# Kernel tuning notes

Hardware: AMD Instinct MI355X
Metric: run time of the kernel (lower is better)

Reference implementation:

```python
import jax, jax.numpy as jnp
import numpy as np

D_MODEL = 1024
H = 16
DH = 64
FFN = 4096
CHUNK = 64
LN_EPS = 1e-5


def layer_norm(x, w, b):
    mu = x.mean(-1, keepdims=True)
    var = x.var(-1, keepdims=True)
    return (x - mu) * jax.lax.rsqrt(var + LN_EPS) * w + b


def l2_normalize(x):
    # matches torch F.normalize(p=2, dim=-1, eps=1e-12)
    n = jnp.sqrt(jnp.sum(x * x, axis=-1, keepdims=True))
    return x / jnp.maximum(n, 1e-12)


def chunk_gla(q, k, v, alpha, C=CHUNK):
    B, Hh, N, D = q.shape
    nc = N // C  # N chosen as multiple of C (pad==0 in original)
    q = q.reshape(B, Hh, nc, C, D)
    k = k.reshape(B, Hh, nc, C, D)
    v = v.reshape(B, Hh, nc, C, D)
    alpha = alpha.reshape(B, Hh, nc, C, D)

    log_a = jnp.log(jnp.maximum(alpha, 1e-6))
    la_cum = jnp.cumsum(log_a, axis=3)                  # (B,H,nc,C,D)
    la_mean = la_cum.mean(-1)                            # (B,H,nc,C)
    tril = jnp.tril(jnp.ones((C, C), dtype=q.dtype))
    decay = jnp.exp(la_mean[..., :, None] - la_mean[..., None, :]) * tril  # (B,H,nc,C,C)

    attn_intra = jnp.einsum('bhncd,bhnmd->bhncm', q, k) * decay
    o_intra = jnp.einsum('bhncm,bhnmd->bhncd', attn_intra, v)

    decay_to_end = jnp.exp(la_cum[:, :, :, -1:, :] - la_cum)
    kv_chunk = jnp.einsum('bhncf,bhnce->bhnfe', k * decay_to_end, v)  # (B,H,nc,D,D)
    chunk_decay = jnp.exp(log_a.sum(3))                  # (B,H,nc,D)
    q_dec = q * jnp.exp(la_cum)                          # decay_from_start

    def step(S, inp):
        qd, kv, cd = inp                                 # (B,H,C,D),(B,H,D,D),(B,H,D)
        o = jnp.einsum('bhcd,bhde->bhce', qd, S)
        S_new = S * cd[:, :, :, None] + kv
        return S_new, o

    S0 = jnp.zeros((B, Hh, D, D), dtype=q.dtype)
    _, o_inter = jax.lax.scan(
        step, S0,
        (jnp.moveaxis(q_dec, 2, 0), jnp.moveaxis(kv_chunk, 2, 0), jnp.moveaxis(chunk_decay, 2, 0)))
    o_inter = jnp.moveaxis(o_inter, 0, 2)                # (B,H,nc,C,D)
    return (o_intra + o_inter).reshape(B, Hh, N, D)


def setup_inputs() -> dict:
    key = jax.random.key(0)
    ks = jax.random.split(key, 16)
    s = 0.02
    td = H * DH
    return {
        'x': jax.random.normal(ks[0], (2, 4096, D_MODEL), dtype=jnp.float32),
        'Wq': jax.random.normal(ks[1], (D_MODEL, td), dtype=jnp.float32) * s,
        'Wk': jax.random.normal(ks[2], (D_MODEL, td), dtype=jnp.float32) * s,
        'Wv': jax.random.normal(ks[3], (D_MODEL, td), dtype=jnp.float32) * s,
        'Wg': jax.random.normal(ks[4], (D_MODEL, td), dtype=jnp.float32) * s,
        'bg': jnp.full((td,), -0.5, dtype=jnp.float32),
        'Wo': jax.random.normal(ks[5], (td, D_MODEL), dtype=jnp.float32) * s,
        'ln1_w': jnp.ones((D_MODEL,), jnp.float32),
        'ln1_b': jnp.zeros((D_MODEL,), jnp.float32),
        'ln2_w': jnp.ones((D_MODEL,), jnp.float32),
        'ln2_b': jnp.zeros((D_MODEL,), jnp.float32),
        'W1': jax.random.normal(ks[6], (D_MODEL, FFN), dtype=jnp.float32) * s,
        'b1': jnp.zeros((FFN,), jnp.float32),
        'W2': jax.random.normal(ks[7], (FFN, D_MODEL), dtype=jnp.float32) * s,
        'b2': jnp.zeros((D_MODEL,), jnp.float32),
    }


def reference(x, Wq, Wk, Wv, Wg, bg, Wo, ln1_w, ln1_b, ln2_w, ln2_b, W1, b1, W2, b2):
    B, N, _ = x.shape
    xn = layer_norm(x, ln1_w, ln1_b)
    q = (xn @ Wq).reshape(B, N, H, DH).transpose(0, 2, 1, 3)
    k = (xn @ Wk).reshape(B, N, H, DH).transpose(0, 2, 1, 3)
    v = (xn @ Wv).reshape(B, N, H, DH).transpose(0, 2, 1, 3)
    q = l2_normalize(q)
    k = l2_normalize(k)
    alpha = jax.nn.sigmoid(xn @ Wg + bg).reshape(B, N, H, DH).transpose(0, 2, 1, 3)
    o = chunk_gla(q, k, v, alpha)
    o = o.transpose(0, 2, 1, 3).reshape(B, N, H * DH)
    x = x + o @ Wo  # dropout off (eval / p=0)
    h = layer_norm(x, ln2_w, ln2_b)
    x = x + jax.nn.gelu(h @ W1 + b1, approximate=False) @ W2 + b2
    return x
```

## Files before the change

kernel.cpp:

```cpp
#include <hip/hip_runtime.h>

#define AS1 __attribute__((address_space(1)))
#define AS3 __attribute__((address_space(3)))

typedef unsigned short u16;
typedef short s16x8 __attribute__((ext_vector_type(8)));
typedef float f32x4 __attribute__((ext_vector_type(4)));
typedef float f32x16 __attribute__((ext_vector_type(16)));

__device__ __forceinline__ float bf2f(u16 u) {
    union { unsigned u; float f; } v; v.u = ((unsigned)u) << 16; return v.f;
}
__device__ __forceinline__ u16 f2bf(float f) {
    union { float f; unsigned u; } v; v.f = f;
    unsigned u = v.u;
    return (u16)((u + 0x7FFFu + ((u >> 16) & 1u)) >> 16);
}

__device__ __forceinline__ void gload16(const void* g, void* l) {
    __builtin_amdgcn_global_load_lds((const AS1 void*)g, (AS3 void*)l, 16, 0, 0);
}

__global__ __launch_bounds__(256) void transpose_bf16(
    const float* __restrict__ src, u16* __restrict__ dst, int R, int C)
{
    __shared__ float t[32][33];
    const int tx = threadIdx.x, ty = threadIdx.y;
    const int r0 = blockIdx.x * 32, c0 = blockIdx.y * 32;
#pragma unroll
    for (int i = 0; i < 4; i++)
        t[ty + i * 8][tx] = src[(size_t)(r0 + ty + i * 8) * C + c0 + tx];
    __syncthreads();
#pragma unroll
    for (int i = 0; i < 4; i++)
        dst[(size_t)(c0 + ty + i * 8) * R + r0 + tx] = f2bf(t[tx][ty + i * 8]);
}

__global__ __launch_bounds__(256) void ln_bf16(
    const float* __restrict__ x, const float* __restrict__ w,
    const float* __restrict__ b, u16* __restrict__ out)
{
    __shared__ float red[8];
    const int row = blockIdx.x;
    const int tid = threadIdx.x;
    const size_t base = (size_t)row * 1024 + tid * 4;
    const float4 xv = *(const float4*)&x[base];
    float s = xv.x + xv.y + xv.z + xv.w;
    float q = xv.x * xv.x + xv.y * xv.y + xv.z * xv.z + xv.w * xv.w;
#pragma unroll
    for (int m = 1; m < 64; m <<= 1) { s += __shfl_xor(s, m); q += __shfl_xor(q, m); }
    if ((tid & 63) == 0) { red[tid >> 6] = s; red[4 + (tid >> 6)] = q; }
    __syncthreads();
    s = red[0] + red[1] + red[2] + red[3];
    q = red[4] + red[5] + red[6] + red[7];
    const float mu = s * (1.f / 1024.f);
    const float var = q * (1.f / 1024.f) - mu * mu;
    const float rs = rsqrtf(var + 1e-5f);
    const float4 wv = *(const float4*)&w[tid * 4];
    const float4 bv = *(const float4*)&b[tid * 4];
    uint2 ov;
    ov.x = (unsigned)f2bf((xv.x - mu) * rs * wv.x + bv.x) |
           ((unsigned)f2bf((xv.y - mu) * rs * wv.y + bv.y) << 16);
    ov.y = (unsigned)f2bf((xv.z - mu) * rs * wv.z + bv.z) |
           ((unsigned)f2bf((xv.w - mu) * rs * wv.w + bv.w) << 16);
    *(uint2*)&out[base] = ov;
}

template <int EPX>
__global__ __launch_bounds__(256, 4) void gemm32(
    const u16* __restrict__ A, const u16* __restrict__ BT,
    float* __restrict__ Cf, u16* __restrict__ Cb,
    const float* __restrict__ bias, const float* __restrict__ resid,
    int M, int N, int K)
{
    __shared__ u16 As[2][4096];
    __shared__ u16 Bs[2][4096];
    const int tid = threadIdx.x;
    const int w = tid >> 6, l = tid & 63;
    const int tm = blockIdx.x * 128, tn = blockIdx.y * 128;
    const int wm = (w >> 1) * 64, wn = (w & 1) * 64;

    const int srow = l >> 2;
    const int sg = ((l & 3) ^ ((l >> 3) & 3)) * 8;
    size_t aSb[2], bSb[2];
#pragma unroll
    for (int j = 0; j < 2; j++) {
        aSb[j] = (size_t)(tm + w * 32 + j * 16 + srow) * K + sg;
        bSb[j] = (size_t)(tn + w * 32 + j * 16 + srow) * K + sg;
    }

    auto stage = [&](int t, int buf) {
        const int k0 = t * 32;
#pragma unroll
        for (int j = 0; j < 2; j++)
            gload16(&A[aSb[j] + k0], &As[buf][(w * 32 + j * 16) * 32]);
#pragma unroll
        for (int j = 0; j < 2; j++)
            gload16(&BT[bSb[j] + k0], &Bs[buf][(w * 32 + j * 16) * 32]);
    };

    const int hi = l >> 5;
    int aoff[2][2], boff[2][2];
#pragma unroll
    for (int mm = 0; mm < 2; mm++)
#pragma unroll
        for (int ks = 0; ks < 2; ks++) {
            const int ra = wm + mm * 32 + (l & 31);
            const int rb = wn + mm * 32 + (l & 31);
            const int key = ((l & 31) >> 1) & 3;
            aoff[mm][ks] = ra * 32 + ((ks * 2 + hi) ^ key) * 8;
            boff[mm][ks] = rb * 32 + ((ks * 2 + hi) ^ key) * 8;
        }

    f32x16 acc[2][2] = {};

    stage(0, 0);
    stage(1, 1);
    asm volatile("s_waitcnt vmcnt(4)" ::: "memory");
    __builtin_amdgcn_s_barrier();

    const int NT = K >> 5;
    for (int t = 0; t < NT; ++t) {
        const int buf = t & 1;
        const u16* as = As[buf];
        const u16* bs = Bs[buf];
        s16x8 a[2][2], b[2][2];
#pragma unroll
        for (int mm = 0; mm < 2; mm++)
#pragma unroll
            for (int ks = 0; ks < 2; ks++) {
                a[mm][ks] = *(const s16x8*)&as[aoff[mm][ks]];
                b[mm][ks] = *(const s16x8*)&bs[boff[mm][ks]];
            }
        asm volatile("s_waitcnt lgkmcnt(0)" ::: "memory");
        __builtin_amdgcn_sched_barrier(0);
        __builtin_amdgcn_s_barrier();
        const bool st = (t + 2 < NT);
        if (st) stage(t + 2, buf);
        __builtin_amdgcn_s_setprio(1);
#pragma unroll
        for (int ks = 0; ks < 2; ks++)
#pragma unroll
            for (int mm = 0; mm < 2; mm++)
#pragma unroll
                for (int nn = 0; nn < 2; nn++)
                    acc[mm][nn] = __builtin_amdgcn_mfma_f32_32x32x16_bf16(
                        a[mm][ks], b[nn][ks], acc[mm][nn], 0, 0, 0);
        __builtin_amdgcn_s_setprio(0);
        if (st)              asm volatile("s_waitcnt vmcnt(4)" ::: "memory");
        else if (t + 1 < NT) asm volatile("s_waitcnt vmcnt(0)" ::: "memory");
        __builtin_amdgcn_s_barrier();
    }

#pragma unroll
    for (int mm = 0; mm < 2; mm++)
#pragma unroll
        for (int nn = 0; nn < 2; nn++)
#pragma unroll
            for (int reg = 0; reg < 16; reg++) {
                const int row = tm + wm + mm * 32 + (l >> 5) * 4 + (reg & 3) + (reg >> 2) * 8;
                const int col = tn + wn + nn * 32 + (l & 31);
                const float v = acc[mm][nn][reg];
                if (EPX == 0) {
                    if (col < 3072) Cb[(size_t)row * 3072 + col] = f2bf(v);
                    else            Cf[(size_t)row * 1024 + (col - 3072)] = v;
                } else if (EPX == 1) {
                    const float u2 = v + bias[col];
                    Cb[(size_t)row * N + col] =
                        f2bf(0.5f * u2 * (1.f + erff(u2 * 0.70710678118654752f)));
                } else if (EPX == 2) {
                    const size_t idx = (size_t)row * N + col;
                    Cf[idx] = v + resid[idx];
                } else {
                    const size_t idx = (size_t)row * N + col;
                    Cf[idx] = v + bias[col] + resid[idx];
                }
            }
}

#define TP 72
#define LP 65
__global__ __launch_bounds__(256) void gla_a(
    const u16* __restrict__ qkv,
    const float* __restrict__ g,
    const float* __restrict__ bg,
    u16* __restrict__ qdec,
    u16* __restrict__ kvT,
    float* __restrict__ cdec,
    u16* __restrict__ ointra)
{
    __shared__ u16 Qh[64 * TP];
    __shared__ u16 Kh[64 * TP];
    __shared__ u16 VT[64 * TP];
    __shared__ float L[64 * LP];
    __shared__ float lm[64], nq[64], nk[64];

    const int bid = blockIdx.x;
    const int bh = bid >> 6, ck = bid & 63;
    const int b = bh >> 4, h = bh & 15;
    const int tok0 = b * 4096 + ck * 64;
    const int tid = threadIdx.x;
    const int w = tid >> 6, l = tid & 63;

#pragma unroll
    for (int pass = 0; pass < 2; pass++) {
        const int c = (tid >> 3) + pass * 32;
        const int col = (tid & 7) * 8;
        const size_t rb = (size_t)(tok0 + c) * 3072 + h * 64 + col;
        uint4 qv = *(const uint4*)&qkv[rb];
        uint4 kv_ = *(const uint4*)&qkv[rb + 1024];
        uint4 vv = *(const uint4*)&qkv[rb + 2048];
        *(uint4*)&Qh[c * TP + col] = qv;
        *(uint4*)&Kh[c * TP + col] = kv_;
        const u16* va = (const u16*)&vv;
#pragma unroll
        for (int j = 0; j < 8; j++) VT[(col + j) * TP + c] = va[j];
    }
#pragma unroll
    for (int pass = 0; pass < 4; pass++) {
        const int c = (tid >> 4) + pass * 16;
        const int col = (tid & 15) * 4;
        float4 gv = *(const float4*)&g[(size_t)(tok0 + c) * 1024 + h * 64 + col];
        float4 bgv = *(const float4*)&bg[h * 64 + col];
        const float* ga = (const float*)&gv;
        const float* ba = (const float*)&bgv;
#pragma unroll
        for (int i = 0; i < 4; i++) {
            const float z = ga[i] + ba[i];
            const float al = 1.f / (1.f + __expf(-z));
            L[c * LP + col + i] = __logf(fmaxf(al, 1e-6f));
        }
    }
    __syncthreads();

    {
        const int d = tid >> 2, qq = tid & 3;
        float vals[16];
#pragma unroll
        for (int i = 0; i < 16; i++) vals[i] = L[(qq * 16 + i) * LP + d];
        float s = 0.f;
#pragma unroll
        for (int i = 0; i < 16; i++) { s += vals[i]; vals[i] = s; }
        float sum = s;
        float u1 = __shfl_up(sum, 1, 4); if (qq >= 1) sum += u1;
        float u2 = __shfl_up(sum, 2, 4); if (qq >= 2) sum += u2;
        const float excl = sum - s;
#pragma unroll
        for (int i = 0; i < 16; i++) L[(qq * 16 + i) * LP + d] = vals[i] + excl;
        if (qq == 3) cdec[((size_t)bh * 64 + ck) * 64 + d] = __expf(sum);
    }
    __syncthreads();

    {
        const int c = tid >> 2, qq = tid & 3;
        float sl = 0.f, sq = 0.f, sk = 0.f;
        uint4 qa = *(const uint4*)&Qh[c * TP + qq * 16];
        uint4 qb = *(const uint4*)&Qh[c * TP + qq * 16 + 8];
        uint4 ka = *(const uint4*)&Kh[c * TP + qq * 16];
        uint4 kb = *(const uint4*)&Kh[c * TP + qq * 16 + 8];
        const u16* qu = (const u16*)&qa; const u16* qu2 = (const u16*)&qb;
        const u16* ku = (const u16*)&ka; const u16* ku2 = (const u16*)&kb;
#pragma unroll
        for (int i = 0; i < 8; i++) {
            float q1 = bf2f(qu[i]), q2 = bf2f(qu2[i]);
            float k1 = bf2f(ku[i]), k2 = bf2f(ku2[i]);
            sq += q1 * q1 + q2 * q2;
            sk += k1 * k1 + k2 * k2;
        }
#pragma unroll
        for (int i = 0; i < 16; i++) sl += L[c * LP + qq * 16 + i];
        sl += __shfl_xor(sl, 1); sl += __shfl_xor(sl, 2);
        sq += __shfl_xor(sq, 1); sq += __shfl_xor(sq, 2);
        sk += __shfl_xor(sk, 1); sk += __shfl_xor(sk, 2);
        if (qq == 0) {
            lm[c] = sl * (1.f / 64.f);
            nq[c] = 1.f / fmaxf(sqrtf(sq), 1e-12f);
            nk[c] = 1.f / fmaxf(sqrtf(sk), 1e-12f);
        }
    }
    __syncthreads();

    u16 kdt[16];
    {
        const int c = tid >> 2, qq = tid & 3;
        const float qn = nq[c], kn = nk[c];
        uint4 qa = *(const uint4*)&Qh[c * TP + qq * 16];
        uint4 qb = *(const uint4*)&Qh[c * TP + qq * 16 + 8];
        uint4 ka = *(const uint4*)&Kh[c * TP + qq * 16];
        uint4 kb = *(const uint4*)&Kh[c * TP + qq * 16 + 8];
        u16* qu = (u16*)&qa; u16* qu2 = (u16*)&qb;
        u16* ku = (u16*)&ka; u16* ku2 = (u16*)&kb;
        float Lc[16], Le[16];
#pragma unroll
        for (int i = 0; i < 16; i++) {
            Lc[i] = L[c * LP + qq * 16 + i];
            Le[i] = L[63 * LP + qq * 16 + i];
        }
        unsigned pk[8];
#pragma unroll
        for (int i = 0; i < 8; i++) {
            float qh1 = bf2f(qu[i]) * qn;  qu[i] = f2bf(qh1);
            float qh2 = bf2f(qu2[i]) * qn; qu2[i] = f2bf(qh2);
            float kh1 = bf2f(ku[i]) * kn;  ku[i] = f2bf(kh1);
            float kh2 = bf2f(ku2[i]) * kn; ku2[i] = f2bf(kh2);
            kdt[i]     = f2bf(kh1 * __expf(Le[i] - Lc[i]));
            kdt[i + 8] = f2bf(kh2 * __expf(Le[i + 8] - Lc[i + 8]));
        }
#pragma unroll
        for (int i = 0; i < 4; i++) {
            pk[i] = (unsigned)f2bf(bf2f(qu[2 * i]) * __expf(Lc[2 * i])) |
                    ((unsigned)f2bf(bf2f(qu[2 * i + 1]) * __expf(Lc[2 * i + 1])) << 16);
            pk[4 + i] = (unsigned)f2bf(bf2f(qu2[2 * i]) * __expf(Lc[8 + 2 * i])) |
                        ((unsigned)f2bf(bf2f(qu2[2 * i + 1]) * __expf(Lc[8 + 2 * i + 1])) << 16);
        }
        *(uint4*)&Qh[c * TP + qq * 16] = qa;
        *(uint4*)&Qh[c * TP + qq * 16 + 8] = qb;
        *(uint4*)&Kh[c * TP + qq * 16] = ka;
        *(uint4*)&Kh[c * TP + qq * 16 + 8] = kb;
        u16* qrow = &qdec[((size_t)bh * 4096 + ck * 64 + c) * 64 + qq * 16];
        *(uint4*)&qrow[0] = *(const uint4*)&pk[0];
        *(uint4*)&qrow[8] = *(const uint4*)&pk[4];
    }
    __syncthreads();

    u16* KDT = (u16*)L;
    {
        const int c = tid >> 2, qq = tid & 3;
#pragma unroll
        for (int i = 0; i < 16; i++) KDT[(qq * 16 + i) * TP + c] = kdt[i];
    }
    const int fr = l & 15;
    const int kk = (l >> 4) * 8;
    f32x4 accS[4] = {};
#pragma unroll
    for (int ks = 0; ks < 2; ks++) {
        s16x8 af = *(const s16x8*)&Qh[(w * 16 + fr) * TP + ks * 32 + kk];
#pragma unroll
        for (int j = 0; j < 4; j++) {
            s16x8 bf = *(const s16x8*)&Kh[(j * 16 + fr) * TP + ks * 32 + kk];
            accS[j] = __builtin_amdgcn_mfma_f32_16x16x32_bf16(af, bf, accS[j], 0, 0, 0);
        }
    }
    __syncthreads();

    {
        const int erow = w * 16 + (l >> 4) * 4;
#pragma unroll
        for (int j = 0; j < 4; j++) {
            const int mm = j * 16 + (l & 15);
            const float lmm = lm[mm];
#pragma unroll
            for (int r = 0; r < 4; r++) {
                const int cc = erow + r;
                const float wgt = (mm <= cc) ? __expf(lm[cc] - lmm) : 0.f;
                Qh[cc * TP + mm] = f2bf(accS[j][r] * wgt);
            }
        }
    }
    __syncthreads();

    f32x4 accO[4] = {};
    f32x4 accK[4] = {};
#pragma unroll
    for (int ks = 0; ks < 2; ks++) {
        s16x8 aAt = *(const s16x8*)&Qh[(w * 16 + fr) * TP + ks * 32 + kk];
        s16x8 aVt = *(const s16x8*)&VT[(w * 16 + fr) * TP + ks * 32 + kk];
#pragma unroll
        for (int j = 0; j < 4; j++) {
            s16x8 bVt = *(const s16x8*)&VT[(j * 16 + fr) * TP + ks * 32 + kk];
            s16x8 bKd = *(const s16x8*)&KDT[(j * 16 + fr) * TP + ks * 32 + kk];
            accO[j] = __builtin_amdgcn_mfma_f32_16x16x32_bf16(aAt, bVt, accO[j], 0, 0, 0);
            accK[j] = __builtin_amdgcn_mfma_f32_16x16x32_bf16(aVt, bKd, accK[j], 0, 0, 0);
        }
    }
    {
        const int erow = w * 16 + (l >> 4) * 4;
#pragma unroll
        for (int j = 0; j < 4; j++) {
            const int col = j * 16 + (l & 15);
#pragma unroll
            for (int r = 0; r < 4; r++) {
                const int row = erow + r;
                ointra[((size_t)bh * 4096 + ck * 64 + row) * 64 + col] = f2bf(accO[j][r]);
                kvT[(((size_t)bh * 64 + ck) * 64 + row) * 64 + col] = f2bf(accK[j][r]);
            }
        }
    }
}

__global__ __launch_bounds__(256) void gla_scan(
    const u16* __restrict__ kvT, const float* __restrict__ cdec,
    u16* __restrict__ ST)
{
    const int bh = blockIdx.x >> 4;
    const int de = (blockIdx.x & 15) * 256 + threadIdx.x;
    const int d = de & 63;
    float s = 0.f;
    const size_t base = (size_t)bh * 64 * 4096 + de;
    const size_t cb = (size_t)bh * 4096 + d;
    for (int t = 0; t < 64; t++) {
        ST[base + (size_t)t * 4096] = f2bf(s);
        s = s * cdec[cb + (size_t)t * 64] + bf2f(kvT[base + (size_t)t * 4096]);
    }
}

__global__ __launch_bounds__(256) void gla_b(
    const u16* __restrict__ qdec, const u16* __restrict__ ST,
    const u16* __restrict__ ointra, u16* __restrict__ obf)
{
    __shared__ u16 Qd[64 * TP];
    __shared__ u16 Sd[64 * TP];
    const int bid = blockIdx.x;
    const int bh = bid >> 6, ck = bid & 63;
    const int b = bh >> 4, h = bh & 15;
    const int tid = threadIdx.x;
    const int w = tid >> 6, l = tid & 63;
#pragma unroll
    for (int pass = 0; pass < 2; pass++) {
        const int r = (tid >> 3) + pass * 32;
        const int col = (tid & 7) * 8;
        *(uint4*)&Qd[r * TP + col] =
            *(const uint4*)&qdec[((size_t)bh * 4096 + ck * 64 + r) * 64 + col];
        *(uint4*)&Sd[r * TP + col] =
            *(const uint4*)&ST[(((size_t)bh * 64 + ck) * 64 + r) * 64 + col];
    }
    __syncthreads();
    const int fr = l & 15;
    const int kk = (l >> 4) * 8;
    f32x4 acc[4] = {};
#pragma unroll
    for (int ks = 0; ks < 2; ks++) {
        s16x8 af = *(const s16x8*)&Qd[(w * 16 + fr) * TP + ks * 32 + kk];
#pragma unroll
        for (int j = 0; j < 4; j++) {
            s16x8 bf = *(const s16x8*)&Sd[(j * 16 + fr) * TP + ks * 32 + kk];
            acc[j] = __builtin_amdgcn_mfma_f32_16x16x32_bf16(af, bf, acc[j], 0, 0, 0);
        }
    }
    const int erow = w * 16 + (l >> 4) * 4;
#pragma unroll
    for (int j = 0; j < 4; j++) {
        const int e = j * 16 + (l & 15);
#pragma unroll
        for (int r = 0; r < 4; r++) {
            const int cc = erow + r;
            const size_t ia = ((size_t)bh * 4096 + ck * 64 + cc) * 64 + e;
            const float v = acc[j][r] + bf2f(ointra[ia]);
            obf[(size_t)(b * 4096 + ck * 64 + cc) * 1024 + h * 64 + e] = f2bf(v);
        }
    }
}

__global__ void fill_sentinel(float* out, int n) {
    int i = blockIdx.x * 256 + threadIdx.x;
    if (i < n) out[i] = 12345.0f;
}

extern "C" void kernel_launch(void* const* d_in, const int* in_sizes, int n_in,
                              void* d_out, int out_size, void* d_ws, size_t ws_size,
                              hipStream_t stream)
{
    const float* x    = (const float*)d_in[0];
    const float* Wq   = (const float*)d_in[1];
    const float* Wk   = (const float*)d_in[2];
    const float* Wv   = (const float*)d_in[3];
    const float* Wg   = (const float*)d_in[4];
    const float* bg   = (const float*)d_in[5];
    const float* Wo   = (const float*)d_in[6];
    const float* ln1w = (const float*)d_in[7];
    const float* ln1b = (const float*)d_in[8];
    const float* ln2w = (const float*)d_in[9];
    const float* ln2b = (const float*)d_in[10];
    const float* W1   = (const float*)d_in[11];
    const float* b1   = (const float*)d_in[12];
    const float* W2   = (const float*)d_in[13];
    const float* b2   = (const float*)d_in[14];
    float* out = (float*)d_out;

    char* ws = (char*)d_ws;
    u16*   wtQKVG = (u16*)(ws + 0);
    u16*   wtWo   = (u16*)(ws + 8388608);
    u16*   wtW1   = (u16*)(ws + 10485760);
    u16*   wtW2   = (u16*)(ws + 18874368);
    u16*   xnb    = (u16*)(ws + 27262976);
    u16*   qkvb   = (u16*)(ws + 44040192);
    float* gbuf   = (float*)(ws + 94371840);
    u16*   kvT    = (u16*)(ws + 127926272);
    float* cdbuf  = (float*)(ws + 144703488);
    u16*   qdecb  = (u16*)(ws + 145227776);
    u16*   ointra = (u16*)(ws + 162004992);
    u16*   STb    = (u16*)(ws + 178782208);
    u16*   obf    = (u16*)(ws + 195559424);
    u16*   hbf    = (u16*)(ws + 212336640);
    float* x2     = (float*)(ws + 94371840);
    u16*   ffnb   = (u16*)(ws + 27262976);

    if (ws_size < 229113856u) {
        fill_sentinel<<<dim3((out_size + 255) / 256), dim3(256), 0, stream>>>(out, out_size);
        return;
    }

    const dim3 b256(256), b32x8(32, 8);

    transpose_bf16<<<dim3(32, 32),  b32x8, 0, stream>>>(Wq, wtQKVG,               1024, 1024);
    transpose_bf16<<<dim3(32, 32),  b32x8, 0, stream>>>(Wk, wtQKVG + 1024 * 1024, 1024, 1024);
    transpose_bf16<<<dim3(32, 32),  b32x8, 0, stream>>>(Wv, wtQKVG + 2048 * 1024, 1024, 1024);
    transpose_bf16<<<dim3(32, 32),  b32x8, 0, stream>>>(Wg, wtQKVG + 3072 * 1024, 1024, 1024);
    transpose_bf16<<<dim3(32, 32),  b32x8, 0, stream>>>(Wo, wtWo,                 1024, 1024);
    transpose_bf16<<<dim3(32, 128), b32x8, 0, stream>>>(W1, wtW1,                 1024, 4096);
    transpose_bf16<<<dim3(128, 32), b32x8, 0, stream>>>(W2, wtW2,                 4096, 1024);

    ln_bf16<<<dim3(8192), b256, 0, stream>>>(x, ln1w, ln1b, xnb);
    gemm32<0><<<dim3(64, 32), b256, 0, stream>>>(xnb, wtQKVG, gbuf, qkvb, nullptr, nullptr, 8192, 4096, 1024);

    gla_a<<<dim3(2048), b256, 0, stream>>>(qkvb, gbuf, bg, qdecb, kvT, cdbuf, ointra);
    gla_scan<<<dim3(512), b256, 0, stream>>>(kvT, cdbuf, STb);
    gla_b<<<dim3(2048), b256, 0, stream>>>(qdecb, STb, ointra, obf);

    gemm32<2><<<dim3(64, 8), b256, 0, stream>>>(obf, wtWo, x2, nullptr, nullptr, x, 8192, 1024, 1024);
    ln_bf16<<<dim3(8192), b256, 0, stream>>>(x2, ln2w, ln2b, hbf);
    gemm32<1><<<dim3(64, 32), b256, 0, stream>>>(hbf, wtW1, nullptr, ffnb, b1, nullptr, 8192, 4096, 1024);
    gemm32<4><<<dim3(64, 8), b256, 0, stream>>>(ffnb, wtW2, out, nullptr, b2, x2, 8192, 1024, 4096);
}
```

Baseline: 423.2 us.

## Replace double-buffered BK32 GEMM with single-buffer BK64 and swizzled block order

Rewrites the bf16 MFMA GEMM to use one 64-wide K tile per iteration in a single LDS buffer, replacing the two 32-wide double buffers. It uses an 8-way XOR swizzle and remaps block IDs so that consecutive blocks spread across the grid for better L2 reuse. The main loop becomes a simple load, sync, compute, sync pattern that halves the number of barriers per K, drops the custom waitcnt and priority scheduling, and lowers the occupancy hint to 3. The risk is that global loads for the next tile are no longer overlapped with compute on a separate buffer, so memory latency may be exposed.

```diff
diff --git a/kernel.cpp b/kernel.cpp
--- a/kernel.cpp
+++ b/kernel.cpp
@@ -67,89 +67,77 @@
 }
 
 template <int EPX>
-__global__ __launch_bounds__(256, 4) void gemm32(
+__global__ __launch_bounds__(256, 3) void gemmS(
     const u16* __restrict__ A, const u16* __restrict__ BT,
     float* __restrict__ Cf, u16* __restrict__ Cb,
     const float* __restrict__ bias, const float* __restrict__ resid,
     int M, int N, int K)
 {
-    __shared__ u16 As[2][4096];
-    __shared__ u16 Bs[2][4096];
+    __shared__ u16 As[8192];
+    __shared__ u16 Bs[8192];
     const int tid = threadIdx.x;
     const int w = tid >> 6, l = tid & 63;
-    const int tm = blockIdx.x * 128, tn = blockIdx.y * 128;
+
+    const int gx = gridDim.x;
+    const int nb = gx * gridDim.y;
+    const int bid0 = blockIdx.y * gx + blockIdx.x;
+    const int swz = (bid0 & 7) * (nb >> 3) + (bid0 >> 3);
+    const int tm = (swz % gx) * 128;
+    const int tn = (swz / gx) * 128;
+
     const int wm = (w >> 1) * 64, wn = (w & 1) * 64;
 
-    const int srow = l >> 2;
-    const int sg = ((l & 3) ^ ((l >> 3) & 3)) * 8;
-    size_t aSb[2], bSb[2];
-#pragma unroll
-    for (int j = 0; j < 2; j++) {
-        aSb[j] = (size_t)(tm + w * 32 + j * 16 + srow) * K + sg;
-        bSb[j] = (size_t)(tn + w * 32 + j * 16 + srow) * K + sg;
-    }
-
-    auto stage = [&](int t, int buf) {
-        const int k0 = t * 32;
-#pragma unroll
-        for (int j = 0; j < 2; j++)
-            gload16(&A[aSb[j] + k0], &As[buf][(w * 32 + j * 16) * 32]);
-#pragma unroll
-        for (int j = 0; j < 2; j++)
-            gload16(&BT[bSb[j] + k0], &Bs[buf][(w * 32 + j * 16) * 32]);
-    };
-
-    const int hi = l >> 5;
-    int aoff[2][2], boff[2][2];
+    const int srow = l >> 3;
+    const int sg = ((l & 7) ^ srow) * 8;
+    size_t aSb[4], bSb[4];
+#pragma unroll
+    for (int j = 0; j < 4; j++) {
+        aSb[j] = (size_t)(tm + j * 32 + w * 8 + srow) * K + sg;
+        bSb[j] = (size_t)(tn + j * 32 + w * 8 + srow) * K + sg;
+    }
+
+    const int la = l & 31, hi = l >> 5, key = l & 7;
+    int aoff[2][4], boff[2][4];
 #pragma unroll
     for (int mm = 0; mm < 2; mm++)
 #pragma unroll
-        for (int ks = 0; ks < 2; ks++) {
-            const int ra = wm + mm * 32 + (l & 31);
-            const int rb = wn + mm * 32 + (l & 31);
-            const int key = ((l & 31) >> 1) & 3;
-            aoff[mm][ks] = ra * 32 + ((ks * 2 + hi) ^ key) * 8;
-            boff[mm][ks] = rb * 32 + ((ks * 2 + hi) ^ key) * 8;
+        for (int ks = 0; ks < 4; ks++) {
+            const int g = ((ks * 2 + hi) ^ key) * 8;
+            aoff[mm][ks] = (wm + mm * 32 + la) * 64 + g;
+            boff[mm][ks] = (wn + mm * 32 + la) * 64 + g;
         }
 
     f32x16 acc[2][2] = {};
 
-    stage(0, 0);
-    stage(1, 1);
-    asm volatile("s_waitcnt vmcnt(4)" ::: "memory");
-    __builtin_amdgcn_s_barrier();
-
-    const int NT = K >> 5;
+#pragma unroll
+    for (int j = 0; j < 4; j++) {
+        gload16(&A[aSb[j]], &As[(j * 32 + w * 8) * 64]);
+        gload16(&BT[bSb[j]], &Bs[(j * 32 + w * 8) * 64]);
+    }
+
+    const int NT = K >> 6;
     for (int t = 0; t < NT; ++t) {
-        const int buf = t & 1;
-        const u16* as = As[buf];
-        const u16* bs = Bs[buf];
-        s16x8 a[2][2], b[2][2];
-#pragma unroll
-        for (int mm = 0; mm < 2; mm++)
-#pragma unroll
-            for (int ks = 0; ks < 2; ks++) {
-                a[mm][ks] = *(const s16x8*)&as[aoff[mm][ks]];
-                b[mm][ks] = *(const s16x8*)&bs[boff[mm][ks]];
+        __syncthreads();
+#pragma unroll
+        for (int ks = 0; ks < 4; ks++) {
+            s16x8 a0 = *(const s16x8*)&As[aoff[0][ks]];
+            s16x8 a1 = *(const s16x8*)&As[aoff[1][ks]];
+            s16x8 b0 = *(const s16x8*)&Bs[boff[0][ks]];
+            s16x8 b1 = *(const s16x8*)&Bs[boff[1][ks]];
+            acc[0][0] = __builtin_amdgcn_mfma_f32_32x32x16_bf16(a0, b0, acc[0][0], 0, 0, 0);
+            acc[0][1] = __builtin_amdgcn_mfma_f32_32x32x16_bf16(a0, b1, acc[0][1], 0, 0, 0);
+            acc[1][0] = __builtin_amdgcn_mfma_f32_32x32x16_bf16(a1, b0, acc[1][0], 0, 0, 0);
+            acc[1][1] = __builtin_amdgcn_mfma_f32_32x32x16_bf16(a1, b1, acc[1][1], 0, 0, 0);
+        }
+        if (t + 1 < NT) {
+            __syncthreads();
+            const int k0 = (t + 1) * 64;
+#pragma unroll
+            for (int j = 0; j < 4; j++) {
+                gload16(&A[aSb[j] + k0], &As[(j * 32 + w * 8) * 64]);
+                gload16(&BT[bSb[j] + k0], &Bs[(j * 32 + w * 8) * 64]);
             }
-        asm volatile("s_waitcnt lgkmcnt(0)" ::: "memory");
-        __builtin_amdgcn_sched_barrier(0);
-        __builtin_amdgcn_s_barrier();
-        const bool st = (t + 2 < NT);
-        if (st) stage(t + 2, buf);
-        __builtin_amdgcn_s_setprio(1);
-#pragma unroll
-        for (int ks = 0; ks < 2; ks++)
-#pragma unroll
-            for (int mm = 0; mm < 2; mm++)
-#pragma unroll
-                for (int nn = 0; nn < 2; nn++)
-                    acc[mm][nn] = __builtin_amdgcn_mfma_f32_32x32x16_bf16(
-                        a[mm][ks], b[nn][ks], acc[mm][nn], 0, 0, 0);
-        __builtin_amdgcn_s_setprio(0);
-        if (st)              asm volatile("s_waitcnt vmcnt(4)" ::: "memory");
-        else if (t + 1 < NT) asm volatile("s_waitcnt vmcnt(0)" ::: "memory");
-        __builtin_amdgcn_s_barrier();
+        }
     }
 
 #pragma unroll
@@ -158,8 +146,8 @@
         for (int nn = 0; nn < 2; nn++)
 #pragma unroll
             for (int reg = 0; reg < 16; reg++) {
-                const int row = tm + wm + mm * 32 + (l >> 5) * 4 + (reg & 3) + (reg >> 2) * 8;
-                const int col = tn + wn + nn * 32 + (l & 31);
+                const int row = tm + wm + mm * 32 + hi * 4 + (reg & 3) + (reg >> 2) * 8;
+                const int col = tn + wn + nn * 32 + la;
                 const float v = acc[mm][nn][reg];
                 if (EPX == 0) {
                     if (col < 3072) Cb[(size_t)row * 3072 + col] = f2bf(v);
@@ -511,14 +499,14 @@
     transpose_bf16<<<dim3(128, 32), b32x8, 0, stream>>>(W2, wtW2,                 4096, 1024);
 
     ln_bf16<<<dim3(8192), b256, 0, stream>>>(x, ln1w, ln1b, xnb);
-    gemm32<0><<<dim3(64, 32), b256, 0, stream>>>(xnb, wtQKVG, gbuf, qkvb, nullptr, nullptr, 8192, 4096, 1024);
+    gemmS<0><<<dim3(64, 32), b256, 0, stream>>>(xnb, wtQKVG, gbuf, qkvb, nullptr, nullptr, 8192, 4096, 1024);
 
     gla_a<<<dim3(2048), b256, 0, stream>>>(qkvb, gbuf, bg, qdecb, kvT, cdbuf, ointra);
     gla_scan<<<dim3(512), b256, 0, stream>>>(kvT, cdbuf, STb);
     gla_b<<<dim3(2048), b256, 0, stream>>>(qdecb, STb, ointra, obf);
 
-    gemm32<2><<<dim3(64, 8), b256, 0, stream>>>(obf, wtWo, x2, nullptr, nullptr, x, 8192, 1024, 1024);
+    gemmS<2><<<dim3(64, 8), b256, 0, stream>>>(obf, wtWo, x2, nullptr, nullptr, x, 8192, 1024, 1024);
     ln_bf16<<<dim3(8192), b256, 0, stream>>>(x2, ln2w, ln2b, hbf);
-    gemm32<1><<<dim3(64, 32), b256, 0, stream>>>(hbf, wtW1, nullptr, ffnb, b1, nullptr, 8192, 4096, 1024);
-    gemm32<4><<<dim3(64, 8), b256, 0, stream>>>(ffnb, wtW2, out, nullptr, b2, x2, 8192, 1024, 4096);
-}
+    gemmS<1><<<dim3(64, 32), b256, 0, stream>>>(hbf, wtW1, nullptr, ffnb, b1, nullptr, 8192, 4096, 1024);
+    gemmS<4><<<dim3(64, 8), b256, 0, stream>>>(ffnb, wtW2, out, nullptr, b2, x2, 8192, 1024, 4096);
+}
```

After: 454.3 us. 7.4% more time.
